# Kernel optimization log

Hardware: AMD Instinct MI355X
Metric: run time of the kernel (lower is better)

## Reference

```python
import jax, jax.numpy as jnp
import numpy as np

# static config
B, T, D, E, K = 2, 2048, 1024, 8, 2
CAPACITY_FACTOR = 1.25
NT = B * T  # num_tokens
_cap = K * NT / E * CAPACITY_FACTOR
_cap += _cap % 2
EXP_CAP = int(_cap)  # 1280


def setup_inputs() -> dict:
    key = jax.random.key(0)
    k1, k2 = jax.random.split(key)
    x = jax.random.normal(k1, (B, T, D), dtype=jnp.float32)
    w_router = jax.random.normal(k2, (E, D), dtype=jnp.float32) * 0.02
    return {"x": x, "w_router": w_router}


def reference(x, w_router):
    # router logits: (B,T,E)
    logits = jnp.einsum('btd,ed->bte', x, w_router)

    # top-k selection
    topk_logits, topk_idx = jax.lax.top_k(logits, K)  # (B,T,K)

    # softmax over only the top-k logits (others masked to -inf), matching
    # torch's full_like(-inf).scatter_(topk) then softmax
    in_topk = jax.nn.one_hot(topk_idx, E, dtype=logits.dtype).sum(axis=-2) > 0  # (B,T,E)
    masked = jnp.where(in_topk, logits, -jnp.inf)
    router_probs = jax.nn.softmax(masked, axis=-1)  # (B,T,E)

    # expert assignment mask: (K, NT, E)
    exp_mask = jax.nn.one_hot(topk_idx, E, dtype=jnp.int32)  # (B,T,K,E)
    exp_mask = exp_mask.reshape(NT, K, E).transpose(1, 0, 2)

    # rank of each token within its expert's buffer (priority: k=0 tokens first)
    rank = jnp.cumsum(exp_mask.reshape(K * NT, E), axis=0) - 1
    rank = rank.reshape(K, NT, E)

    # drop tokens that exceed expert capacity
    exp_mask = exp_mask * (rank < EXP_CAP).astype(jnp.int32)
    used_cap = jnp.sum(exp_mask, axis=(0, 1))  # (E,)

    # per-(k, token) slot index within the assigned expert's buffer
    slot = jnp.sum(exp_mask * rank, axis=-1)  # (K, NT) int

    probs_flat = router_probs.reshape(NT, E)
    exp_weights = exp_mask.astype(probs_flat.dtype) * probs_flat[None]  # (K,NT,E)

    # cb_weight[t, e, c] = sum_k exp_weights[k,t,e] * (slot[k,t] == c)
    # scatter-add instead of materializing the one-hot (K,NT,EXP_CAP) tensor
    t_idx = jnp.broadcast_to(jnp.arange(NT)[None, :], (K, NT))
    cb_weight = jnp.zeros((NT, E, EXP_CAP), dtype=probs_flat.dtype)
    cb_weight = cb_weight.at[t_idx, :, slot].add(exp_weights)  # (NT,E,EXP_CAP)

    sec_mask = cb_weight != 0  # bool dispatch mask
    return used_cap, cb_weight, sec_mask
```

## Files before the change

### kernel.cpp

```cpp
#include <hip/hip_runtime.h>
#include <hip/hip_bf16.h>
#include <math.h>

#define NT      4096
#define DD      1024
#define EE      8
#define KK      2
#define CAP     1280
#define CBN     (NT * EE * CAP)
#define NROW    (NT * EE)
#define F4ROW   (CAP / 4)
#define VROWS   (2 * NROW)

__device__ __forceinline__ int swz(int j) { return j ^ ((j >> 5) & 31); }

__global__ __launch_bounds__(256) void logits_kernel(
    const float* __restrict__ x,
    const float* __restrict__ w,
    int* __restrict__ e0, int* __restrict__ e1,
    float* __restrict__ p0, float* __restrict__ p1)
{
    __shared__ float wl[EE * DD];

    for (int i = threadIdx.x; i < EE * DD / 4; i += 256)
        reinterpret_cast<float4*>(wl)[i] = reinterpret_cast<const float4*>(w)[i];
    __syncthreads();

    const int wave = threadIdx.x >> 6;
    const int lane = threadIdx.x & 63;
    const int wid  = blockIdx.x * 4 + wave;

    for (int t = wid; t < NT; t += gridDim.x * 4) {
        const float4* xt = reinterpret_cast<const float4*>(x + (size_t)t * DD);
        float acc[EE];
        #pragma unroll
        for (int e = 0; e < EE; ++e) acc[e] = 0.0f;

        #pragma unroll
        for (int ii = 0; ii < DD / 4 / 64; ++ii) {
            const int i = ii * 64 + lane;
            const float4 xv = xt[i];
            #pragma unroll
            for (int e = 0; e < EE; ++e) {
                const float4 wv = reinterpret_cast<const float4*>(wl + e * DD)[i];
                acc[e] += xv.x * wv.x + xv.y * wv.y + xv.z * wv.z + xv.w * wv.w;
            }
        }

        #pragma unroll
        for (int e = 0; e < EE; ++e) {
            float v = acc[e];
            #pragma unroll
            for (int off = 32; off > 0; off >>= 1) v += __shfl_xor(v, off);
            acc[e] = v;
        }

        if (lane == 0) {
            int b0 = 0; float l0 = acc[0];
            #pragma unroll
            for (int e = 1; e < EE; ++e) { if (acc[e] > l0) { l0 = acc[e]; b0 = e; } }
            int b1 = -1; float l1 = -INFINITY;
            #pragma unroll
            for (int e = 0; e < EE; ++e) { if (e != b0 && acc[e] > l1) { l1 = acc[e]; b1 = e; } }

            const float z  = expf(l1 - l0);
            const float pa = 1.0f / (1.0f + z);
            const float pb = z * pa;

            e0[t] = b0; e1[t] = b1;
            p0[t] = pa; p1[t] = pb;
        }
    }
}

__global__ __launch_bounds__(256) void rank_table_kernel(
    const int* __restrict__ e0, const int* __restrict__ e1,
    const float* __restrict__ p0, const float* __restrict__ p1,
    int* __restrict__ sl, float* __restrict__ val,
    float* __restrict__ out)
{
    __shared__ int   se[KK * NT];
    __shared__ float sp[KK * NT];
    __shared__ unsigned long long wsumA[4], wsumB[4];

    const int tid = threadIdx.x;

    int4* sl4 = reinterpret_cast<int4*>(sl);
    const int4 neg = make_int4(-1, -1, -1, -1);
    for (int i = tid; i < NROW / 4; i += 256) sl4[i] = neg;

    for (int i = tid; i < NT; i += 256) {
        se[swz(i)]      = e0[i];
        se[swz(NT + i)] = e1[i];
        sp[swz(i)]      = p0[i];
        sp[swz(NT + i)] = p1[i];
    }
    __syncthreads();

    const int base = tid * 32;
    unsigned long long ca = 0ull, cb = 0ull;
    #pragma unroll
    for (int i = 0; i < 32; ++i) {
        const int e = se[swz(base + i)];
        if (e < 4) ca += 1ull << (16 * e);
        else       cb += 1ull << (16 * (e - 4));
    }

    unsigned long long sa = ca, sb = cb;
    #pragma unroll
    for (int off = 1; off < 64; off <<= 1) {
        const unsigned long long ta = __shfl_up(sa, off);
        const unsigned long long tb = __shfl_up(sb, off);
        if ((tid & 63) >= off) { sa += ta; sb += tb; }
    }
    const int wv = tid >> 6;
    if ((tid & 63) == 63) { wsumA[wv] = sa; wsumB[wv] = sb; }
    __syncthreads();

    unsigned long long preA = 0ull, preB = 0ull;
    #pragma unroll
    for (int k = 0; k < 4; ++k) {
        if (k < wv) { preA += wsumA[k]; preB += wsumB[k]; }
    }
    unsigned long long ra = preA + sa - ca;
    unsigned long long rb = preB + sb - cb;

    #pragma unroll
    for (int i = 0; i < 32; ++i) {
        const int j = base + i;
        const int e = se[swz(j)];
        int rank;
        if (e < 4) { rank = (int)((ra >> (16 * e)) & 0xFFFF);       ra += 1ull << (16 * e); }
        else       { rank = (int)((rb >> (16 * (e - 4))) & 0xFFFF); rb += 1ull << (16 * (e - 4)); }
        if (rank < CAP) {
            const int t = j & (NT - 1);
            sl[t * EE + e]  = rank;
            val[t * EE + e] = sp[swz(j)];
        }
    }

    if (tid < EE) {
        const unsigned long long totA = wsumA[0] + wsumA[1] + wsumA[2] + wsumA[3];
        const unsigned long long totB = wsumB[0] + wsumB[1] + wsumB[2] + wsumB[3];
        const int e = tid;
        const int tot = (e < 4) ? (int)((totA >> (16 * e)) & 0xFFFF)
                                : (int)((totB >> (16 * (e - 4))) & 0xFFFF);
        out[e] = (float)((tot < CAP) ? tot : CAP);
    }
}

__global__ __launch_bounds__(256) void write_kernel(
    const int* __restrict__ sl, const float* __restrict__ val,
    float* __restrict__ out)
{
    const int wid  = (blockIdx.x << 2) + (threadIdx.x >> 6);
    const int lane = threadIdx.x & 63;
    float4* base = reinterpret_cast<float4*>(out + 8);

    #pragma unroll
    for (int rr = 0; rr < 4; ++rr) {
        const int vr = (wid << 2) + rr;
        const int r  = __builtin_amdgcn_readfirstlane(vr & (NROW - 1));
        const int   s = sl[r];
        const float p = val[r];
        const bool  on = (s >= 0) && (p != 0.0f);
        const float hv = (vr >= NROW) ? 1.0f : p;

        float4* dst = base + (size_t)vr * F4ROW;
        #pragma unroll
        for (int it = 0; it < 5; ++it) {
            const int f4 = (it << 6) + lane;
            const int c  = f4 << 2;
            float4 v;
            v.x = (on && s == c)     ? hv : 0.0f;
            v.y = (on && s == c + 1) ? hv : 0.0f;
            v.z = (on && s == c + 2) ? hv : 0.0f;
            v.w = (on && s == c + 3) ? hv : 0.0f;
            dst[f4] = v;
        }
    }
}

extern "C" void kernel_launch(void* const* d_in, const int* in_sizes, int n_in,
                              void* d_out, int out_size, void* d_ws, size_t ws_size,
                              hipStream_t stream) {
    const float* x = (const float*)d_in[0];
    const float* w = (const float*)d_in[1];
    float* out = (float*)d_out;

    char* ws = (char*)d_ws;
    int*   e0  = (int*)(ws);
    int*   e1  = (int*)(ws + 16 * 1024);
    float* p0  = (float*)(ws + 32 * 1024);
    float* p1  = (float*)(ws + 48 * 1024);
    int*   sl  = (int*)(ws + 64 * 1024);
    float* val = (float*)(ws + 192 * 1024);

    logits_kernel<<<256, 256, 0, stream>>>(x, w, e0, e1, p0, p1);

    rank_table_kernel<<<1, 256, 0, stream>>>(e0, e1, p0, p1, sl, val, out);

    write_kernel<<<4096, 256, 0, stream>>>(sl, val, out);
}
```

Measured before the change: 96.36 us.

## Fuse logits, rank, and write kernels into one persistent kernel with grid barriers

Merges the three launches into a single persistent kernel of 256 blocks, using an atomic-counter grid barrier between the logits phase, the single-block rank scan, and the dense output write. The goal is to remove the launch gaps and tail effects between kernels. In exchange, the write phase now runs on only 256 blocks, each handling 64 rows per wave instead of being spread over 4096 blocks, which may reduce memory-level parallelism. It also adds a memset and spin-wait barriers that assume all blocks are co-resident.

```diff
diff --git a/kernel.cpp b/kernel.cpp
--- a/kernel.cpp
+++ b/kernel.cpp
@@ -10,27 +10,48 @@
 #define CBN     (NT * EE * CAP)
 #define NROW    (NT * EE)
 #define F4ROW   (CAP / 4)
-#define VROWS   (2 * NROW)
+
+#define NB      256
+#define NWAVES  (NB * 4)
+#define RPW     (2 * NROW / NWAVES)
 
 __device__ __forceinline__ int swz(int j) { return j ^ ((j >> 5) & 31); }
 
-__global__ __launch_bounds__(256) void logits_kernel(
+__device__ __forceinline__ void gridbar(unsigned* cnt, unsigned target) {
+    __syncthreads();
+    if (threadIdx.x == 0) {
+        __hip_atomic_fetch_add(cnt, 1u, __ATOMIC_ACQ_REL, __HIP_MEMORY_SCOPE_AGENT);
+        while (__hip_atomic_load(cnt, __ATOMIC_ACQUIRE, __HIP_MEMORY_SCOPE_AGENT) < target)
+            __builtin_amdgcn_s_sleep(2);
+    }
+    __syncthreads();
+}
+
+__global__ __launch_bounds__(256) void fused_router_kernel(
     const float* __restrict__ x,
     const float* __restrict__ w,
+    float* __restrict__ out,
+    unsigned* __restrict__ cnt,
     int* __restrict__ e0, int* __restrict__ e1,
-    float* __restrict__ p0, float* __restrict__ p1)
+    float* __restrict__ p0, float* __restrict__ p1,
+    int* __restrict__ sl, float* __restrict__ val)
 {
-    __shared__ float wl[EE * DD];
-
-    for (int i = threadIdx.x; i < EE * DD / 4; i += 256)
-        reinterpret_cast<float4*>(wl)[i] = reinterpret_cast<const float4*>(w)[i];
+    __shared__ union {
+        float wl[EE * DD];
+        struct { int se[KK * NT]; float sp[KK * NT]; } s2;
+    } u;
+    __shared__ unsigned long long wsumA[4], wsumB[4];
+
+    const int tid  = threadIdx.x;
+    const int wave = tid >> 6;
+    const int lane = tid & 63;
+
+    for (int i = tid; i < EE * DD / 4; i += 256)
+        reinterpret_cast<float4*>(u.wl)[i] = reinterpret_cast<const float4*>(w)[i];
     __syncthreads();
 
-    const int wave = threadIdx.x >> 6;
-    const int lane = threadIdx.x & 63;
-    const int wid  = blockIdx.x * 4 + wave;
-
-    for (int t = wid; t < NT; t += gridDim.x * 4) {
+    const int wid = blockIdx.x * 4 + wave;
+    for (int t = wid; t < NT; t += NWAVES) {
         const float4* xt = reinterpret_cast<const float4*>(x + (size_t)t * DD);
         float acc[EE];
         #pragma unroll
@@ -42,7 +63,7 @@
             const float4 xv = xt[i];
             #pragma unroll
             for (int e = 0; e < EE; ++e) {
-                const float4 wv = reinterpret_cast<const float4*>(wl + e * DD)[i];
+                const float4 wv = reinterpret_cast<const float4*>(u.wl + e * DD)[i];
                 acc[e] += xv.x * wv.x + xv.y * wv.y + xv.z * wv.z + xv.w * wv.w;
             }
         }
@@ -71,102 +92,87 @@
             p0[t] = pa; p1[t] = pb;
         }
     }
-}
-
-__global__ __launch_bounds__(256) void rank_table_kernel(
-    const int* __restrict__ e0, const int* __restrict__ e1,
-    const float* __restrict__ p0, const float* __restrict__ p1,
-    int* __restrict__ sl, float* __restrict__ val,
-    float* __restrict__ out)
-{
-    __shared__ int   se[KK * NT];
-    __shared__ float sp[KK * NT];
-    __shared__ unsigned long long wsumA[4], wsumB[4];
-
-    const int tid = threadIdx.x;
-
-    int4* sl4 = reinterpret_cast<int4*>(sl);
-    const int4 neg = make_int4(-1, -1, -1, -1);
-    for (int i = tid; i < NROW / 4; i += 256) sl4[i] = neg;
-
-    for (int i = tid; i < NT; i += 256) {
-        se[swz(i)]      = e0[i];
-        se[swz(NT + i)] = e1[i];
-        sp[swz(i)]      = p0[i];
-        sp[swz(NT + i)] = p1[i];
-    }
-    __syncthreads();
-
-    const int base = tid * 32;
-    unsigned long long ca = 0ull, cb = 0ull;
-    #pragma unroll
-    for (int i = 0; i < 32; ++i) {
-        const int e = se[swz(base + i)];
-        if (e < 4) ca += 1ull << (16 * e);
-        else       cb += 1ull << (16 * (e - 4));
-    }
-
-    unsigned long long sa = ca, sb = cb;
-    #pragma unroll
-    for (int off = 1; off < 64; off <<= 1) {
-        const unsigned long long ta = __shfl_up(sa, off);
-        const unsigned long long tb = __shfl_up(sb, off);
-        if ((tid & 63) >= off) { sa += ta; sb += tb; }
-    }
-    const int wv = tid >> 6;
-    if ((tid & 63) == 63) { wsumA[wv] = sa; wsumB[wv] = sb; }
-    __syncthreads();
-
-    unsigned long long preA = 0ull, preB = 0ull;
-    #pragma unroll
-    for (int k = 0; k < 4; ++k) {
-        if (k < wv) { preA += wsumA[k]; preB += wsumB[k]; }
-    }
-    unsigned long long ra = preA + sa - ca;
-    unsigned long long rb = preB + sb - cb;
-
-    #pragma unroll
-    for (int i = 0; i < 32; ++i) {
-        const int j = base + i;
-        const int e = se[swz(j)];
-        int rank;
-        if (e < 4) { rank = (int)((ra >> (16 * e)) & 0xFFFF);       ra += 1ull << (16 * e); }
-        else       { rank = (int)((rb >> (16 * (e - 4))) & 0xFFFF); rb += 1ull << (16 * (e - 4)); }
-        if (rank < CAP) {
-            const int t = j & (NT - 1);
-            sl[t * EE + e]  = rank;
-            val[t * EE + e] = sp[swz(j)];
-        }
-    }
-
-    if (tid < EE) {
-        const unsigned long long totA = wsumA[0] + wsumA[1] + wsumA[2] + wsumA[3];
-        const unsigned long long totB = wsumB[0] + wsumB[1] + wsumB[2] + wsumB[3];
-        const int e = tid;
-        const int tot = (e < 4) ? (int)((totA >> (16 * e)) & 0xFFFF)
-                                : (int)((totB >> (16 * (e - 4))) & 0xFFFF);
-        out[e] = (float)((tot < CAP) ? tot : CAP);
-    }
-}
-
-__global__ __launch_bounds__(256) void write_kernel(
-    const int* __restrict__ sl, const float* __restrict__ val,
-    float* __restrict__ out)
-{
-    const int wid  = (blockIdx.x << 2) + (threadIdx.x >> 6);
-    const int lane = threadIdx.x & 63;
-    float4* base = reinterpret_cast<float4*>(out + 8);
-
-    #pragma unroll
-    for (int rr = 0; rr < 4; ++rr) {
-        const int vr = (wid << 2) + rr;
+
+    gridbar(cnt, NB);
+
+    if (blockIdx.x == 0) {
+        int4* sl4 = reinterpret_cast<int4*>(sl);
+        const int4 neg = make_int4(-1, -1, -1, -1);
+        for (int i = tid; i < NROW / 4; i += 256) sl4[i] = neg;
+
+        for (int i = tid; i < NT; i += 256) {
+            u.s2.se[swz(i)]      = e0[i];
+            u.s2.se[swz(NT + i)] = e1[i];
+            u.s2.sp[swz(i)]      = p0[i];
+            u.s2.sp[swz(NT + i)] = p1[i];
+        }
+        __syncthreads();
+
+        const int base = tid * 32;
+        unsigned long long ca = 0ull, cb = 0ull;
+        #pragma unroll
+        for (int i = 0; i < 32; ++i) {
+            const int e = u.s2.se[swz(base + i)];
+            if (e < 4) ca += 1ull << (16 * e);
+            else       cb += 1ull << (16 * (e - 4));
+        }
+
+        unsigned long long sa = ca, sb = cb;
+        #pragma unroll
+        for (int off = 1; off < 64; off <<= 1) {
+            const unsigned long long ta = __shfl_up(sa, off);
+            const unsigned long long tb = __shfl_up(sb, off);
+            if ((tid & 63) >= off) { sa += ta; sb += tb; }
+        }
+        if ((tid & 63) == 63) { wsumA[wave] = sa; wsumB[wave] = sb; }
+        __syncthreads();
+
+        unsigned long long preA = 0ull, preB = 0ull;
+        #pragma unroll
+        for (int k = 0; k < 4; ++k) {
+            if (k < wave) { preA += wsumA[k]; preB += wsumB[k]; }
+        }
+        unsigned long long ra = preA + sa - ca;
+        unsigned long long rb = preB + sb - cb;
+
+        #pragma unroll
+        for (int i = 0; i < 32; ++i) {
+            const int j = base + i;
+            const int e = u.s2.se[swz(j)];
+            int rank;
+            if (e < 4) { rank = (int)((ra >> (16 * e)) & 0xFFFF);       ra += 1ull << (16 * e); }
+            else       { rank = (int)((rb >> (16 * (e - 4))) & 0xFFFF); rb += 1ull << (16 * (e - 4)); }
+            if (rank < CAP) {
+                const int t = j & (NT - 1);
+                sl[t * EE + e]  = rank;
+                val[t * EE + e] = u.s2.sp[swz(j)];
+            }
+        }
+
+        if (tid < EE) {
+            const unsigned long long totA = wsumA[0] + wsumA[1] + wsumA[2] + wsumA[3];
+            const unsigned long long totB = wsumB[0] + wsumB[1] + wsumB[2] + wsumB[3];
+            const int e = tid;
+            const int tot = (e < 4) ? (int)((totA >> (16 * e)) & 0xFFFF)
+                                    : (int)((totB >> (16 * (e - 4))) & 0xFFFF);
+            out[e] = (float)((tot < CAP) ? tot : CAP);
+        }
+    }
+
+    gridbar(cnt, 2 * NB);
+
+    const int gw = blockIdx.x * 4 + wave;
+    float4* base4 = reinterpret_cast<float4*>(out + 8);
+
+    for (int rr = 0; rr < RPW; ++rr) {
+        const int vr = gw * RPW + rr;
         const int r  = __builtin_amdgcn_readfirstlane(vr & (NROW - 1));
         const int   s = sl[r];
         const float p = val[r];
         const bool  on = (s >= 0) && (p != 0.0f);
         const float hv = (vr >= NROW) ? 1.0f : p;
 
-        float4* dst = base + (size_t)vr * F4ROW;
+        float4* dst = base4 + (size_t)vr * F4ROW;
         #pragma unroll
         for (int it = 0; it < 5; ++it) {
             const int f4 = (it << 6) + lane;
@@ -189,16 +195,15 @@
     float* out = (float*)d_out;
 
     char* ws = (char*)d_ws;
-    int*   e0  = (int*)(ws);
-    int*   e1  = (int*)(ws + 16 * 1024);
-    float* p0  = (float*)(ws + 32 * 1024);
-    float* p1  = (float*)(ws + 48 * 1024);
-    int*   sl  = (int*)(ws + 64 * 1024);
-    float* val = (float*)(ws + 192 * 1024);
-
-    logits_kernel<<<256, 256, 0, stream>>>(x, w, e0, e1, p0, p1);
-
-    rank_table_kernel<<<1, 256, 0, stream>>>(e0, e1, p0, p1, sl, val, out);
-
-    write_kernel<<<4096, 256, 0, stream>>>(sl, val, out);
+    unsigned* cnt = (unsigned*)(ws);
+    int*   e0  = (int*)(ws + 1 * 1024);
+    int*   e1  = (int*)(ws + 17 * 1024);
+    float* p0  = (float*)(ws + 33 * 1024);
+    float* p1  = (float*)(ws + 49 * 1024);
+    int*   sl  = (int*)(ws + 72 * 1024);
+    float* val = (float*)(ws + 200 * 1024);
+
+    hipMemsetAsync(cnt, 0, 64, stream);
+
+    fused_router_kernel<<<NB, 256, 0, stream>>>(x, w, out, cnt, e0, e1, p0, p1, sl, val);
 }
```

Measured after the change: 288.9 us. +199.8%, slower.
